# Kernel tuning notes

Measured on AMD Instinct MI355X. Metric: run time of the kernel, lower is better.

Reference implementation:

```python
import jax, jax.numpy as jnp
import numpy as np

NUM_USERS = 50000
NUM_ITEMS = 10000
NUM_SUPPORT = 5
INPUT_DIM = 512
OUTPUT_DIM = 500
NNZ = 400000


def setup_inputs() -> dict:
    key = jax.random.key(0)
    ks = jax.random.split(key, 6)
    x_u = jax.random.normal(ks[0], (NUM_USERS, INPUT_DIM), dtype=jnp.float32)
    x_v = jax.random.normal(ks[1], (NUM_ITEMS, INPUT_DIM), dtype=jnp.float32)
    # random-uniform-like weight init (weight_variable_random_uniform)
    weights_u = jax.random.normal(ks[2], (INPUT_DIM, OUTPUT_DIM), dtype=jnp.float32) * 0.05
    sup_vals = jax.random.uniform(ks[3], (NUM_SUPPORT, NNZ), dtype=jnp.float32)
    sup_rows = jax.random.randint(ks[4], (NUM_SUPPORT, NNZ), 0, NUM_USERS, dtype=jnp.int32)
    sup_cols = jax.random.randint(ks[5], (NUM_SUPPORT, NNZ), 0, NUM_ITEMS, dtype=jnp.int32)
    return {"x_u": x_u, "x_v": x_v, "weights_u": weights_u,
            "sup_vals": sup_vals, "sup_rows": sup_rows, "sup_cols": sup_cols}


def reference(x_u, x_v, weights_u, sup_vals, sup_rows, sup_cols):
    # share_user_item_weights=True -> weights_v is weights_u; dropout=0.0 -> identity.
    hidden = OUTPUT_DIM // NUM_SUPPORT  # 100
    supports_u, supports_v = [], []
    for i in range(NUM_SUPPORT):
        Wi = jax.lax.dynamic_slice_in_dim(weights_u, i * hidden, hidden, axis=1)
        tmp_u = x_u @ Wi  # [num_users, hidden]
        tmp_v = x_v @ Wi  # [num_items, hidden]
        vals = sup_vals[i][:, None]  # [nnz, 1]
        rows, cols = sup_rows[i], sup_cols[i]
        # support_i @ tmp_v  (sparse [U,I] times dense [I,h])
        su = jax.ops.segment_sum(vals * tmp_v[cols], rows, num_segments=NUM_USERS)
        # support_i^T @ tmp_u (sparse [I,U] times dense [U,h])
        sv = jax.ops.segment_sum(vals * tmp_u[rows], cols, num_segments=NUM_ITEMS)
        supports_u.append(su)
        supports_v.append(sv)
    z_u = jnp.concatenate(supports_u, axis=1)  # [num_users, output_dim]
    z_v = jnp.concatenate(supports_v, axis=1)  # [num_items, output_dim]
    return (jax.nn.relu(z_u), jax.nn.relu(z_v))
```

## Files before the change

### kernel.cpp

```cpp
#include <hip/hip_runtime.h>

#define NUM_USERS   50000
#define NUM_ITEMS   10000
#define NUM_SUPPORT 5
#define INPUT_DIM   512
#define OUTPUT_DIM  500
#define NPAD        512
#define HIDDEN      100
#define HPAD        128
#define NNZ         400000
#define NEDGE       (NUM_SUPPORT * NNZ)

#define CH_E        8192
#define NCHUNK      ((NEDGE + CH_E - 1) / CH_E)
#define NB_U        ((NUM_SUPPORT * NUM_USERS + 255) / 256)
#define NB_V        ((NUM_SUPPORT * NUM_ITEMS + 255) / 256)
#define HISTM_U_SZ  (NB_U * NCHUNK)
#define HISTM_U_PAD 239366
#define HISTM_V_SZ  (NB_V * NCHUNK)

typedef unsigned int u32;
typedef unsigned short ushort_t;
typedef __attribute__((ext_vector_type(4))) float f32x4;
typedef __attribute__((ext_vector_type(8))) short bf16x8;

#define GLDS(g, l) __builtin_amdgcn_global_load_lds( \
    (const __attribute__((address_space(1))) unsigned int*)(g), \
    (__attribute__((address_space(3))) unsigned int*)(l), 16, 0, 0)

__device__ inline ushort_t bf16_rne(float f) {
    u32 u = __float_as_uint(f);
    u32 r = (u + 0x7FFFu + ((u >> 16) & 1u)) >> 16;
    return (ushort_t)r;
}
__device__ inline float bf16_lo_f32(u32 w) { return __uint_as_float(w << 16); }
__device__ inline float bf16_hi_f32(u32 w) { return __uint_as_float(w & 0xFFFF0000u); }

__global__ __launch_bounds__(256) void cvt_bf16(
    const float4* __restrict__ in, ushort4* __restrict__ out, int n4)
{
    int t = blockIdx.x * 256 + threadIdx.x;
    if (t >= n4) return;
    float4 v = in[t];
    ushort4 o;
    o.x = bf16_rne(v.x); o.y = bf16_rne(v.y);
    o.z = bf16_rne(v.z); o.w = bf16_rne(v.w);
    out[t] = o;
}

__global__ __launch_bounds__(256) void make_WbT(
    const float* __restrict__ W, ushort_t* __restrict__ WbT)
{
    int t = blockIdx.x * 256 + threadIdx.x;
    int n = t >> 9, k = t & 511;
    float v = (n < OUTPUT_DIM) ? W[k * OUTPUT_DIM + n] : 0.f;
    WbT[t] = bf16_rne(v);
}

#define BM 128
#define BN 128
#define BK 32

__global__ __launch_bounds__(256) void gemm_mfma_bf16(
    const ushort_t* __restrict__ A,
    const ushort_t* __restrict__ BT,
    ushort_t* __restrict__ Xp,
    int M)
{
    const int K = INPUT_DIM;
    __shared__ ushort_t As[BM * BK];
    __shared__ ushort_t Bs[BN * BK];

    const int tid  = threadIdx.x;
    const int wave = tid >> 6;
    const int lane = tid & 63;
    const int quad = lane >> 4;
    const int lr   = lane & 15;
    const int m0 = blockIdx.x * BM;
    const int n0 = blockIdx.y * BN;
    const int wm = (wave >> 1) * 64;
    const int wn = (wave & 1) * 64;

    f32x4 acc[4][4] = {};

    for (int k0 = 0; k0 < K; k0 += BK) {
        #pragma unroll
        for (int h = 0; h < 2; ++h) {
            int o   = tid * 16 + h * 4096;
            int row = o >> 6;
            int byt = o & 63;
            int gr  = m0 + row; if (gr >= M) gr = M - 1;
            GLDS((const char*)A + ((long long)gr * K + k0) * 2 + byt, (char*)As + o);
        }
        #pragma unroll
        for (int h = 0; h < 2; ++h) {
            int o   = tid * 16 + h * 4096;
            int row = o >> 6;
            int byt = o & 63;
            GLDS((const char*)BT + ((long long)(n0 + row) * K + k0) * 2 + byt, (char*)Bs + o);
        }
        asm volatile("s_waitcnt vmcnt(0)" ::: "memory");
        __syncthreads();

        bf16x8 af[4], bfr[4];
        #pragma unroll
        for (int tm = 0; tm < 4; ++tm)
            af[tm] = *(const bf16x8*)(As + (wm + tm * 16 + lr) * BK + quad * 8);
        #pragma unroll
        for (int tn = 0; tn < 4; ++tn)
            bfr[tn] = *(const bf16x8*)(Bs + (wn + tn * 16 + lr) * BK + quad * 8);
        #pragma unroll
        for (int tm = 0; tm < 4; ++tm)
            #pragma unroll
            for (int tn = 0; tn < 4; ++tn)
                acc[tm][tn] = __builtin_amdgcn_mfma_f32_16x16x32_bf16(
                    af[tm], bfr[tn], acc[tm][tn], 0, 0, 0);
        __syncthreads();
    }

    #pragma unroll
    for (int tm = 0; tm < 4; ++tm) {
        int rbase = m0 + wm + tm * 16 + quad * 4;
        #pragma unroll
        for (int tn = 0; tn < 4; ++tn) {
            int col = n0 + wn + tn * 16 + lr;
            if (col >= OUTPUT_DIM) continue;
            int seg = col / HIDDEN;
            int off = col - seg * HIDDEN;
            ushort_t* dst = Xp + (long long)seg * M * HPAD + off;
            #pragma unroll
            for (int g = 0; g < 4; ++g) {
                int row = rbase + g;
                if (row < M) dst[(long long)row * HPAD] = bf16_rne(acc[tm][tn][g]);
            }
        }
    }
}

__global__ __launch_bounds__(256) void scan1(u32* __restrict__ data, int n,
                                             u32* __restrict__ partials)
{
    __shared__ u32 sh[256];
    int t = threadIdx.x;
    int base = blockIdx.x * 1024 + t * 4;
    u32 x[4];
    #pragma unroll
    for (int k = 0; k < 4; ++k) {
        int idx = base + k;
        x[k] = (idx < n) ? data[idx] : 0u;
    }
    u32 tsum = x[0] + x[1] + x[2] + x[3];
    sh[t] = tsum;
    __syncthreads();
    for (int off = 1; off < 256; off <<= 1) {
        u32 v = (t >= off) ? sh[t - off] : 0u;
        __syncthreads();
        sh[t] += v;
        __syncthreads();
    }
    u32 run = (t > 0) ? sh[t - 1] : 0u;
    if (t == 255) partials[blockIdx.x] = sh[255];
    #pragma unroll
    for (int k = 0; k < 4; ++k) {
        int idx = base + k;
        if (idx < n) data[idx] = run;
        run += x[k];
    }
}

__global__ __launch_bounds__(256) void scan_partials(u32* __restrict__ partials, int n)
{
    __shared__ u32 sh[256];
    int t = threadIdx.x;
    u32 x = (t < n) ? partials[t] : 0u;
    sh[t] = x;
    __syncthreads();
    for (int off = 1; off < 256; off <<= 1) {
        u32 v = (t >= off) ? sh[t - off] : 0u;
        __syncthreads();
        sh[t] += v;
        __syncthreads();
    }
    if (t < n) partials[t] = (t > 0) ? sh[t - 1] : 0u;
}

__global__ __launch_bounds__(256) void scan_add(u32* __restrict__ data, int n,
                                                const u32* __restrict__ partials)
{
    int idx = blockIdx.x * 256 + threadIdx.x;
    if (idx < n) data[idx] += partials[idx >> 10];
}

__global__ __launch_bounds__(256) void hist_uv(
    const int* __restrict__ rows, const int* __restrict__ cols,
    u32* __restrict__ histm_u, u32* __restrict__ histm_v)
{
    __shared__ u32 hu[NB_U];
    __shared__ u32 hv[NB_V];
    const int tid = threadIdx.x;
    const int c = blockIdx.x;
    for (int b = tid; b < NB_U; b += 256) hu[b] = 0u;
    for (int b = tid; b < NB_V; b += 256) hv[b] = 0u;
    __syncthreads();
    int base = c * CH_E;
    int end = base + CH_E; if (end > NEDGE) end = NEDGE;
    for (int e = base + tid; e < end; e += 256) {
        unsigned i = (unsigned)e / (unsigned)NNZ;
        u32 ku = i * (u32)NUM_USERS + (u32)rows[e];
        u32 kv = i * (u32)NUM_ITEMS + (u32)cols[e];
        atomicAdd(&hu[ku >> 8], 1u);
        atomicAdd(&hv[kv >> 8], 1u);
    }
    __syncthreads();
    for (int b = tid; b < NB_U; b += 256) histm_u[b * NCHUNK + c] = hu[b];
    for (int b = tid; b < NB_V; b += 256) histm_v[b * NCHUNK + c] = hv[b];
}

template<int NROWS, int GSHIFT>
__global__ __launch_bounds__(256) void partition_edges(
    const int* __restrict__ keyidx, const int* __restrict__ gidx,
    const float* __restrict__ vals,
    const u32* __restrict__ histm, uint2* __restrict__ buf)
{
    constexpr int NKEY = NUM_SUPPORT * NROWS;
    constexpr int NB = (NKEY + 255) / 256;
    __shared__ u32 cur[NB];
    const int tid = threadIdx.x;
    const int c = blockIdx.x;
    for (int b = tid; b < NB; b += 256) cur[b] = histm[b * NCHUNK + c];
    __syncthreads();
    int base = c * CH_E;
    int end = base + CH_E; if (end > NEDGE) end = NEDGE;
    for (int e = base + tid; e < end; e += 256) {
        unsigned i = (unsigned)e / (unsigned)NNZ;
        u32 key = i * (u32)NROWS + (u32)keyidx[e];
        u32 p = atomicAdd(&cur[key >> 8], 1u);
        uint2 pay;
        pay.x = __float_as_uint(vals[e]);
        pay.y = (key << GSHIFT) | (u32)gidx[e];
        buf[p] = pay;
    }
}

template<int NROWS, int GSHIFT>
__global__ __launch_bounds__(256) void bucket_scatter(
    const uint2* __restrict__ buf, const u32* __restrict__ histm,
    u32* __restrict__ ptr, uint2* __restrict__ perm)
{
    constexpr int NKEY = NUM_SUPPORT * NROWS;
    constexpr int NB = (NKEY + 255) / 256;
    __shared__ u32 cnt[256];
    __shared__ u32 scn[256];
    const int tid = threadIdx.x;
    const int b = blockIdx.x;
    const u32 key0 = (u32)b << 8;
    const u32 start = histm[b * NCHUNK];
    const u32 bend  = (b + 1 < NB) ? histm[(b + 1) * NCHUNK] : (u32)NEDGE;
    if (b == 0 && tid == 0) ptr[NKEY] = (u32)NEDGE;
    cnt[tid] = 0u;
    __syncthreads();
    for (u32 j = start + tid; j < bend; j += 256) {
        u32 key = buf[j].y >> GSHIFT;
        atomicAdd(&cnt[key - key0], 1u);
    }
    __syncthreads();
    scn[tid] = cnt[tid];
    __syncthreads();
    for (int off = 1; off < 256; off <<= 1) {
        u32 v = (tid >= off) ? scn[tid - off] : 0u;
        __syncthreads();
        scn[tid] += v;
        __syncthreads();
    }
    u32 myoff = start + scn[tid] - cnt[tid];
    if (key0 + (u32)tid < (u32)NKEY) ptr[key0 + tid] = myoff;
    __syncthreads();
    cnt[tid] = myoff;
    __syncthreads();
    for (u32 j = start + tid; j < bend; j += 256) {
        uint2 q = buf[j];
        u32 key = q.y >> GSHIFT;
        u32 p = atomicAdd(&cnt[key - key0], 1u);
        uint2 out;
        out.x = q.x;
        out.y = q.y & ((1u << GSHIFT) - 1u);
        perm[p] = out;
    }
}

template<int NROWS>
__global__ __launch_bounds__(256) void spmm_pack4(
    const u32* __restrict__ ptr,
    const uint2* __restrict__ perm,
    const ushort_t* __restrict__ Xp,
    float* __restrict__ Z,
    int nsrc)
{
    constexpr int NKEY = NUM_SUPPORT * NROWS;
    int w = (int)((blockIdx.x * 256u + threadIdx.x) >> 6);
    w = __builtin_amdgcn_readfirstlane(w);
    if (w * 4 >= NKEY) return;
    const int lane = threadIdx.x & 63;
    const int g  = lane >> 4;
    const int sl = lane & 15;

    int key = w * 4 + g;
    bool live = key < NKEY;
    int kc = live ? key : (NKEY - 1);
    int i = kc / NROWS;
    int r = kc - i * NROWS;
    u32 s = ptr[kc];
    u32 e = live ? ptr[kc + 1] : s;

    const ushort_t* Xs = Xp + (long long)i * nsrc * HPAD + sl * 8;

    u32 cnt = e - s;
    u32 m = cnt;
    { u32 t = (u32)__shfl_xor((int)m, 16); m = m > t ? m : t; }
    { u32 t = (u32)__shfl_xor((int)m, 32); m = m > t ? m : t; }
    int iters = (int)((m + 1) >> 1);

    float a0 = 0.f, a1 = 0.f, a2 = 0.f, a3 = 0.f;
    float a4 = 0.f, a5 = 0.f, a6 = 0.f, a7 = 0.f;
    u32 k = s;
    for (int it = 0; it < iters; ++it) {
        bool p0 = k < e, p1 = (k + 1) < e;
        u32 j0 = p0 ? k : 0u;
        u32 j1 = p1 ? (k + 1) : 0u;
        uint2 q0 = perm[j0], q1 = perm[j1];
        float v0 = p0 ? __uint_as_float(q0.x) : 0.f;
        float v1 = p1 ? __uint_as_float(q1.x) : 0.f;
        uint4 w0 = *(const uint4*)(Xs + ((long long)q0.y << 7));
        uint4 w1 = *(const uint4*)(Xs + ((long long)q1.y << 7));
        a0 += v0 * bf16_lo_f32(w0.x) + v1 * bf16_lo_f32(w1.x);
        a1 += v0 * bf16_hi_f32(w0.x) + v1 * bf16_hi_f32(w1.x);
        a2 += v0 * bf16_lo_f32(w0.y) + v1 * bf16_lo_f32(w1.y);
        a3 += v0 * bf16_hi_f32(w0.y) + v1 * bf16_hi_f32(w1.y);
        a4 += v0 * bf16_lo_f32(w0.z) + v1 * bf16_lo_f32(w1.z);
        a5 += v0 * bf16_hi_f32(w0.z) + v1 * bf16_hi_f32(w1.z);
        a6 += v0 * bf16_lo_f32(w0.w) + v1 * bf16_lo_f32(w1.w);
        a7 += v0 * bf16_hi_f32(w0.w) + v1 * bf16_hi_f32(w1.w);
        k += 2;
    }

    if (live && sl < 13) {
        float* zp = Z + (long long)r * OUTPUT_DIM + i * HIDDEN + sl * 8;
        float4 o0;
        o0.x = a0 > 0.f ? a0 : 0.f;
        o0.y = a1 > 0.f ? a1 : 0.f;
        o0.z = a2 > 0.f ? a2 : 0.f;
        o0.w = a3 > 0.f ? a3 : 0.f;
        *(float4*)zp = o0;
        if (sl < 12) {
            float4 o1;
            o1.x = a4 > 0.f ? a4 : 0.f;
            o1.y = a5 > 0.f ? a5 : 0.f;
            o1.z = a6 > 0.f ? a6 : 0.f;
            o1.w = a7 > 0.f ? a7 : 0.f;
            *(float4*)(zp + 4) = o1;
        }
    }
}

#define TM 64
#define TN 64
#define TK 16

__global__ __launch_bounds__(256) void gemm_f32(
    const float* __restrict__ A, const float* __restrict__ B,
    float* __restrict__ C, int M, int N, int K, int ldc)
{
    __shared__ float Asl[TK][TM + 4];
    __shared__ float Bsl[TK][TN + 4];
    const int tid = threadIdx.x;
    const int tx  = tid & 15;
    const int ty  = tid >> 4;
    const int row0 = blockIdx.x * TM;
    const int col0 = blockIdx.y * TN;
    float acc[4][4] = {};
    for (int k0 = 0; k0 < K; k0 += TK) {
        #pragma unroll
        for (int it = 0; it < (TM * TK) / 256; ++it) {
            int idx = tid + it * 256;
            int m = idx >> 4, kk = idx & 15, gr = row0 + m;
            Asl[kk][m] = (gr < M) ? A[(long long)gr * K + (k0 + kk)] : 0.f;
        }
        #pragma unroll
        for (int it = 0; it < (TK * TN) / 256; ++it) {
            int idx = tid + it * 256;
            int kk = idx >> 6, n = idx & 63, gc = col0 + n;
            Bsl[kk][n] = (gc < N) ? B[(long long)(k0 + kk) * N + gc] : 0.f;
        }
        __syncthreads();
        #pragma unroll
        for (int kk = 0; kk < TK; ++kk) {
            float a[4], b[4];
            #pragma unroll
            for (int u = 0; u < 4; ++u) a[u] = Asl[kk][ty * 4 + u];
            #pragma unroll
            for (int v = 0; v < 4; ++v) b[v] = Bsl[kk][tx * 4 + v];
            #pragma unroll
            for (int u = 0; u < 4; ++u)
                #pragma unroll
                for (int v = 0; v < 4; ++v)
                    acc[u][v] += a[u] * b[v];
        }
        __syncthreads();
    }
    #pragma unroll
    for (int u = 0; u < 4; ++u) {
        int gr = row0 + ty * 4 + u;
        if (gr >= M) continue;
        #pragma unroll
        for (int v = 0; v < 4; ++v) {
            int gc = col0 + tx * 4 + v;
            if (gc < N) C[(long long)gr * ldc + gc] = acc[u][v];
        }
    }
}

__global__ __launch_bounds__(256) void scatter_edges(
    const float* __restrict__ sup_vals,
    const int*   __restrict__ sup_rows,
    const int*   __restrict__ sup_cols,
    const float* __restrict__ XU, const float* __restrict__ XV,
    float* __restrict__ z_u, float* __restrict__ z_v)
{
    const unsigned t = blockIdx.x * 256u + threadIdx.x;
    const unsigned total = (unsigned)NEDGE * HIDDEN;
    if (t >= total) return;
    const unsigned j  = t % HIDDEN;
    const unsigned eg = t / HIDDEN;
    const unsigned i  = eg / NNZ;
    const float val = sup_vals[eg];
    const int   r   = sup_rows[eg];
    const int   c   = sup_cols[eg];
    const int   colOff = i * HIDDEN + j;
    atomicAdd(&z_u[(long long)r * OUTPUT_DIM + colOff],
              val * XV[(long long)c * NPAD + colOff]);
    atomicAdd(&z_v[(long long)c * OUTPUT_DIM + colOff],
              val * XU[(long long)r * NPAD + colOff]);
}

__global__ __launch_bounds__(256) void relu_inplace(float4* __restrict__ p, int n4)
{
    int t = blockIdx.x * 256 + threadIdx.x;
    if (t >= n4) return;
    float4 v = p[t];
    v.x = v.x > 0.f ? v.x : 0.f;
    v.y = v.y > 0.f ? v.y : 0.f;
    v.z = v.z > 0.f ? v.z : 0.f;
    v.w = v.w > 0.f ? v.w : 0.f;
    p[t] = v;
}

extern "C" void kernel_launch(void* const* d_in, const int* in_sizes, int n_in,
                              void* d_out, int out_size, void* d_ws, size_t ws_size,
                              hipStream_t stream)
{
    const float* x_u      = (const float*)d_in[0];
    const float* x_v      = (const float*)d_in[1];
    const float* W        = (const float*)d_in[2];
    const float* sup_vals = (const float*)d_in[3];
    const int*   sup_rows = (const int*)d_in[4];
    const int*   sup_cols = (const int*)d_in[5];

    float* z_u = (float*)d_out;
    float* z_v = z_u + (long long)NUM_USERS * OUTPUT_DIM;

    const long long NU = (long long)NUM_USERS * 512;
    const long long NV = (long long)NUM_ITEMS * 512;
    const long long PU = (long long)NUM_SUPPORT * NUM_USERS * HPAD;
    const long long PV = (long long)NUM_SUPPORT * NUM_ITEMS * HPAD;
    const int NRU = NUM_SUPPORT * NUM_USERS;
    const int NRV = NUM_SUPPORT * NUM_ITEMS;

    ushort_t* Xp_u  = (ushort_t*)d_ws;
    ushort_t* Xp_v  = Xp_u + PU;
    ushort_t* xu_in = Xp_v + PV;
    ushort_t* xv_in = xu_in + NU;
    ushort_t* WbT   = xv_in + NV;
    u32* row_ptr_u  = (u32*)(WbT + 512 * 512);
    u32* col_ptr_v  = row_ptr_u + (NRU + 1);
    u32* partials   = col_ptr_v + (NRV + 1);
    size_t need_full = ((char*)(partials + 1024)) - ((char*)d_ws);

    uint2* buf      = (uint2*)xu_in;
    u32*   histm_u  = (u32*)(buf + NEDGE);
    u32*   histm_v  = histm_u + HISTM_U_PAD;
    uint2* perm_u   = (uint2*)(histm_v + HISTM_V_SZ);
    uint2* perm_v   = perm_u + NEDGE;

    dim3 blk(256);

    if (ws_size >= need_full) {
        cvt_bf16<<<(int)((NU / 4 + 255) / 256), blk, 0, stream>>>(
            (const float4*)x_u, (ushort4*)xu_in, (int)(NU / 4));
        cvt_bf16<<<(int)((NV / 4 + 255) / 256), blk, 0, stream>>>(
            (const float4*)x_v, (ushort4*)xv_in, (int)(NV / 4));
        make_WbT<<<(512 * 512) / 256, blk, 0, stream>>>(W, WbT);
        gemm_mfma_bf16<<<dim3((NUM_USERS + BM - 1) / BM, 512 / BN), blk, 0, stream>>>(
            xu_in, WbT, Xp_u, NUM_USERS);
        gemm_mfma_bf16<<<dim3((NUM_ITEMS + BM - 1) / BM, 512 / BN), blk, 0, stream>>>(
            xv_in, WbT, Xp_v, NUM_ITEMS);

        auto scan_u32 = [&](u32* data, int n) {
            int nb = (n + 1023) / 1024;
            scan1<<<nb, blk, 0, stream>>>(data, n, partials);
            scan_partials<<<1, blk, 0, stream>>>(partials, nb);
            scan_add<<<(n + 255) / 256, blk, 0, stream>>>(data, n, partials);
        };

        hist_uv<<<NCHUNK, blk, 0, stream>>>(sup_rows, sup_cols, histm_u, histm_v);

        scan_u32(histm_u, HISTM_U_SZ);
        partition_edges<NUM_USERS, 14><<<NCHUNK, blk, 0, stream>>>(
            sup_rows, sup_cols, sup_vals, histm_u, buf);
        bucket_scatter<NUM_USERS, 14><<<NB_U, blk, 0, stream>>>(
            buf, histm_u, row_ptr_u, perm_u);

        scan_u32(histm_v, HISTM_V_SZ);
        partition_edges<NUM_ITEMS, 16><<<NCHUNK, blk, 0, stream>>>(
            sup_cols, sup_rows, sup_vals, histm_v, buf);
        bucket_scatter<NUM_ITEMS, 16><<<NB_V, blk, 0, stream>>>(
            buf, histm_v, col_ptr_v, perm_v);

        spmm_pack4<NUM_USERS><<<((NRU / 4) * 64) / 256, blk, 0, stream>>>(
            row_ptr_u, perm_u, Xp_v, z_u, NUM_ITEMS);
        spmm_pack4<NUM_ITEMS><<<((NRV / 4) * 64) / 256, blk, 0, stream>>>(
            col_ptr_v, perm_v, Xp_u, z_v, NUM_USERS);
    } else {
        float* XU = (float*)d_ws;
        float* XV = XU + (long long)NUM_USERS * NPAD;
        gemm_f32<<<dim3((NUM_USERS + TM - 1) / TM, (OUTPUT_DIM + TN - 1) / TN),
                   blk, 0, stream>>>(x_u, W, XU, NUM_USERS, OUTPUT_DIM, INPUT_DIM, NPAD);
        gemm_f32<<<dim3((NUM_ITEMS + TM - 1) / TM, (OUTPUT_DIM + TN - 1) / TN),
                   blk, 0, stream>>>(x_v, W, XV, NUM_ITEMS, OUTPUT_DIM, INPUT_DIM, NPAD);
        hipMemsetAsync(d_out, 0, (size_t)out_size * sizeof(float), stream);
        unsigned total = (unsigned)NEDGE * HIDDEN;
        scatter_edges<<<(total + 255u) / 256u, blk, 0, stream>>>(
            sup_vals, sup_rows, sup_cols, XU, XV, z_u, z_v);
        int n4 = out_size / 4;
        relu_inplace<<<(n4 + 255) / 256, blk, 0, stream>>>((float4*)d_out, n4);
    }
}
```

Before: 568.3 us.

## Merge user/item sort pipelines into joint scan, partition and scatter kernels

```diff
diff --git a/kernel.cpp b/kernel.cpp
--- a/kernel.cpp
+++ b/kernel.cpp
@@ -16,8 +16,9 @@
 #define NB_U        ((NUM_SUPPORT * NUM_USERS + 255) / 256)
 #define NB_V        ((NUM_SUPPORT * NUM_ITEMS + 255) / 256)
 #define HISTM_U_SZ  (NB_U * NCHUNK)
-#define HISTM_U_PAD 239366
+#define HISTM_U_ALIGN 239616
 #define HISTM_V_SZ  (NB_V * NCHUNK)
+#define HISTM_TOT   (HISTM_U_ALIGN + HISTM_V_SZ)
 
 typedef unsigned int u32;
 typedef unsigned short ushort_t;
@@ -36,16 +37,21 @@
 __device__ inline float bf16_lo_f32(u32 w) { return __uint_as_float(w << 16); }
 __device__ inline float bf16_hi_f32(u32 w) { return __uint_as_float(w & 0xFFFF0000u); }
 
-__global__ __launch_bounds__(256) void cvt_bf16(
-    const float4* __restrict__ in, ushort4* __restrict__ out, int n4)
+__global__ __launch_bounds__(256) void cvt_bf16_2(
+    const float4* __restrict__ a, const float4* __restrict__ b,
+    ushort4* __restrict__ oa, ushort4* __restrict__ ob, int na4, int nb4)
 {
     int t = blockIdx.x * 256 + threadIdx.x;
-    if (t >= n4) return;
-    float4 v = in[t];
+    const float4* src;
+    ushort4* dst;
+    int idx;
+    if (t < na4) { src = a; dst = oa; idx = t; }
+    else { idx = t - na4; if (idx >= nb4) return; src = b; dst = ob; }
+    float4 v = src[idx];
     ushort4 o;
     o.x = bf16_rne(v.x); o.y = bf16_rne(v.y);
     o.z = bf16_rne(v.z); o.w = bf16_rne(v.w);
-    out[t] = o;
+    dst[idx] = o;
 }
 
 __global__ __launch_bounds__(256) void make_WbT(
@@ -168,14 +174,14 @@
     }
 }
 
-__global__ __launch_bounds__(256) void scan_partials(u32* __restrict__ partials, int n)
-{
-    __shared__ u32 sh[256];
+__global__ __launch_bounds__(512) void scan_partials(u32* __restrict__ partials, int n)
+{
+    __shared__ u32 sh[512];
     int t = threadIdx.x;
     u32 x = (t < n) ? partials[t] : 0u;
     sh[t] = x;
     __syncthreads();
-    for (int off = 1; off < 256; off <<= 1) {
+    for (int off = 1; off < 512; off <<= 1) {
         u32 v = (t >= off) ? sh[t - off] : 0u;
         __syncthreads();
         sh[t] += v;
@@ -188,7 +194,9 @@
                                                 const u32* __restrict__ partials)
 {
     int idx = blockIdx.x * 256 + threadIdx.x;
-    if (idx < n) data[idx] += partials[idx >> 10];
+    if (idx >= n) return;
+    u32 adj = (idx >= HISTM_U_ALIGN) ? (u32)NEDGE : 0u;
+    data[idx] = data[idx] + partials[idx >> 10] - adj;
 }
 
 __global__ __launch_bounds__(256) void hist_uv(
@@ -199,6 +207,8 @@
     __shared__ u32 hv[NB_V];
     const int tid = threadIdx.x;
     const int c = blockIdx.x;
+    if (c == 0)
+        for (int z = HISTM_U_SZ + tid; z < HISTM_U_ALIGN; z += 256) histm_u[z] = 0u;
     for (int b = tid; b < NB_U; b += 256) hu[b] = 0u;
     for (int b = tid; b < NB_V; b += 256) hv[b] = 0u;
     __syncthreads();
@@ -216,43 +226,46 @@
     for (int b = tid; b < NB_V; b += 256) histm_v[b * NCHUNK + c] = hv[b];
 }
 
-template<int NROWS, int GSHIFT>
-__global__ __launch_bounds__(256) void partition_edges(
-    const int* __restrict__ keyidx, const int* __restrict__ gidx,
+__global__ __launch_bounds__(256) void partition_uv(
+    const int* __restrict__ rows, const int* __restrict__ cols,
     const float* __restrict__ vals,
-    const u32* __restrict__ histm, uint2* __restrict__ buf)
-{
-    constexpr int NKEY = NUM_SUPPORT * NROWS;
-    constexpr int NB = (NKEY + 255) / 256;
-    __shared__ u32 cur[NB];
+    const u32* __restrict__ histm_u, const u32* __restrict__ histm_v,
+    uint2* __restrict__ buf_u, uint2* __restrict__ buf_v)
+{
+    __shared__ u32 cu[NB_U];
+    __shared__ u32 cv[NB_V];
     const int tid = threadIdx.x;
     const int c = blockIdx.x;
-    for (int b = tid; b < NB; b += 256) cur[b] = histm[b * NCHUNK + c];
+    for (int b = tid; b < NB_U; b += 256) cu[b] = histm_u[b * NCHUNK + c];
+    for (int b = tid; b < NB_V; b += 256) cv[b] = histm_v[b * NCHUNK + c];
     __syncthreads();
     int base = c * CH_E;
     int end = base + CH_E; if (end > NEDGE) end = NEDGE;
     for (int e = base + tid; e < end; e += 256) {
         unsigned i = (unsigned)e / (unsigned)NNZ;
-        u32 key = i * (u32)NROWS + (u32)keyidx[e];
-        u32 p = atomicAdd(&cur[key >> 8], 1u);
-        uint2 pay;
-        pay.x = __float_as_uint(vals[e]);
-        pay.y = (key << GSHIFT) | (u32)gidx[e];
-        buf[p] = pay;
+        int r = rows[e];
+        int col = cols[e];
+        u32 vb = __float_as_uint(vals[e]);
+        u32 ku = i * (u32)NUM_USERS + (u32)r;
+        u32 kv = i * (u32)NUM_ITEMS + (u32)col;
+        u32 pu = atomicAdd(&cu[ku >> 8], 1u);
+        uint2 eu; eu.x = vb; eu.y = (ku << 14) | (u32)col;
+        buf_u[pu] = eu;
+        u32 pv = atomicAdd(&cv[kv >> 8], 1u);
+        uint2 ev; ev.x = vb; ev.y = (kv << 16) | (u32)r;
+        buf_v[pv] = ev;
     }
 }
 
 template<int NROWS, int GSHIFT>
-__global__ __launch_bounds__(256) void bucket_scatter(
-    const uint2* __restrict__ buf, const u32* __restrict__ histm,
-    u32* __restrict__ ptr, uint2* __restrict__ perm)
+__device__ inline void bucket_body(
+    int b, const uint2* __restrict__ buf, const u32* __restrict__ histm,
+    u32* __restrict__ ptr, uint2* __restrict__ perm,
+    u32* cnt, u32* scn)
 {
     constexpr int NKEY = NUM_SUPPORT * NROWS;
     constexpr int NB = (NKEY + 255) / 256;
-    __shared__ u32 cnt[256];
-    __shared__ u32 scn[256];
     const int tid = threadIdx.x;
-    const int b = blockIdx.x;
     const u32 key0 = (u32)b << 8;
     const u32 start = histm[b * NCHUNK];
     const u32 bend  = (b + 1 < NB) ? histm[(b + 1) * NCHUNK] : (u32)NEDGE;
@@ -288,6 +301,20 @@
     }
 }
 
+__global__ __launch_bounds__(256) void bucket_scatter_uv(
+    const uint2* __restrict__ buf_u, const u32* __restrict__ histm_u,
+    u32* __restrict__ ptr_u, uint2* __restrict__ perm_u,
+    const uint2* __restrict__ buf_v, const u32* __restrict__ histm_v,
+    u32* __restrict__ ptr_v, uint2* __restrict__ perm_v)
+{
+    __shared__ u32 cnt[256];
+    __shared__ u32 scn[256];
+    if (blockIdx.x < NB_U)
+        bucket_body<NUM_USERS, 14>(blockIdx.x, buf_u, histm_u, ptr_u, perm_u, cnt, scn);
+    else
+        bucket_body<NUM_ITEMS, 16>(blockIdx.x - NB_U, buf_v, histm_v, ptr_v, perm_v, cnt, scn);
+}
+
 template<int NROWS>
 __global__ __launch_bounds__(256) void spmm_pack4(
     const u32* __restrict__ ptr,
@@ -305,45 +332,56 @@
     const int sl = lane & 15;
 
     int key = w * 4 + g;
-    bool live = key < NKEY;
-    int kc = live ? key : (NKEY - 1);
-    int i = kc / NROWS;
-    int r = kc - i * NROWS;
-    u32 s = ptr[kc];
-    u32 e = live ? ptr[kc + 1] : s;
+    int i = key / NROWS;
+    int r = key - i * NROWS;
+    u32 s = ptr[key];
+    u32 e = ptr[key + 1];
 
     const ushort_t* Xs = Xp + (long long)i * nsrc * HPAD + sl * 8;
 
-    u32 cnt = e - s;
-    u32 m = cnt;
+    u32 m = e - s;
     { u32 t = (u32)__shfl_xor((int)m, 16); m = m > t ? m : t; }
     { u32 t = (u32)__shfl_xor((int)m, 32); m = m > t ? m : t; }
-    int iters = (int)((m + 1) >> 1);
+    int iters = (int)((m + 3) >> 2);
 
     float a0 = 0.f, a1 = 0.f, a2 = 0.f, a3 = 0.f;
     float a4 = 0.f, a5 = 0.f, a6 = 0.f, a7 = 0.f;
     u32 k = s;
     for (int it = 0; it < iters; ++it) {
-        bool p0 = k < e, p1 = (k + 1) < e;
+        bool p0 = k < e, p1 = (k + 1) < e, p2 = (k + 2) < e, p3 = (k + 3) < e;
         u32 j0 = p0 ? k : 0u;
         u32 j1 = p1 ? (k + 1) : 0u;
-        uint2 q0 = perm[j0], q1 = perm[j1];
+        u32 j2 = p2 ? (k + 2) : 0u;
+        u32 j3 = p3 ? (k + 3) : 0u;
+        uint2 q0 = perm[j0], q1 = perm[j1], q2 = perm[j2], q3 = perm[j3];
         float v0 = p0 ? __uint_as_float(q0.x) : 0.f;
         float v1 = p1 ? __uint_as_float(q1.x) : 0.f;
+        float v2 = p2 ? __uint_as_float(q2.x) : 0.f;
+        float v3 = p3 ? __uint_as_float(q3.x) : 0.f;
         uint4 w0 = *(const uint4*)(Xs + ((long long)q0.y << 7));
         uint4 w1 = *(const uint4*)(Xs + ((long long)q1.y << 7));
-        a0 += v0 * bf16_lo_f32(w0.x) + v1 * bf16_lo_f32(w1.x);
-        a1 += v0 * bf16_hi_f32(w0.x) + v1 * bf16_hi_f32(w1.x);
-        a2 += v0 * bf16_lo_f32(w0.y) + v1 * bf16_lo_f32(w1.y);
-        a3 += v0 * bf16_hi_f32(w0.y) + v1 * bf16_hi_f32(w1.y);
-        a4 += v0 * bf16_lo_f32(w0.z) + v1 * bf16_lo_f32(w1.z);
-        a5 += v0 * bf16_hi_f32(w0.z) + v1 * bf16_hi_f32(w1.z);
-        a6 += v0 * bf16_lo_f32(w0.w) + v1 * bf16_lo_f32(w1.w);
-        a7 += v0 * bf16_hi_f32(w0.w) + v1 * bf16_hi_f32(w1.w);
-        k += 2;
-    }
-
-    if (live && sl < 13) {
+        uint4 w2 = *(const uint4*)(Xs + ((long long)q2.y << 7));
+        uint4 w3 = *(const uint4*)(Xs + ((long long)q3.y << 7));
+        a0 += v0 * bf16_lo_f32(w0.x) + v1 * bf16_lo_f32(w1.x)
+            + v2 * bf16_lo_f32(w2.x) + v3 * bf16_lo_f32(w3.x);
+        a1 += v0 * bf16_hi_f32(w0.x) + v1 * bf16_hi_f32(w1.x)
+            + v2 * bf16_hi_f32(w2.x) + v3 * bf16_hi_f32(w3.x);
+        a2 += v0 * bf16_lo_f32(w0.y) + v1 * bf16_lo_f32(w1.y)
+            + v2 * bf16_lo_f32(w2.y) + v3 * bf16_lo_f32(w3.y);
+        a3 += v0 * bf16_hi_f32(w0.y) + v1 * bf16_hi_f32(w1.y)
+            + v2 * bf16_hi_f32(w2.y) + v3 * bf16_hi_f32(w3.y);
+        a4 += v0 * bf16_lo_f32(w0.z) + v1 * bf16_lo_f32(w1.z)
+            + v2 * bf16_lo_f32(w2.z) + v3 * bf16_lo_f32(w3.z);
+        a5 += v0 * bf16_hi_f32(w0.z) + v1 * bf16_hi_f32(w1.z)
+            + v2 * bf16_hi_f32(w2.z) + v3 * bf16_hi_f32(w3.z);
+        a6 += v0 * bf16_lo_f32(w0.w) + v1 * bf16_lo_f32(w1.w)
+            + v2 * bf16_lo_f32(w2.w) + v3 * bf16_lo_f32(w3.w);
+        a7 += v0 * bf16_hi_f32(w0.w) + v1 * bf16_hi_f32(w1.w)
+            + v2 * bf16_hi_f32(w2.w) + v3 * bf16_hi_f32(w3.w);
+        k += 4;
+    }
+
+    if (sl < 13) {
         float* zp = Z + (long long)r * OUTPUT_DIM + i * HIDDEN + sl * 8;
         float4 o0;
         o0.x = a0 > 0.f ? a0 : 0.f;
@@ -483,47 +521,46 @@
     u32* row_ptr_u  = (u32*)(WbT + 512 * 512);
     u32* col_ptr_v  = row_ptr_u + (NRU + 1);
     u32* partials   = col_ptr_v + (NRV + 1);
-    size_t need_full = ((char*)(partials + 1024)) - ((char*)d_ws);
-
-    uint2* buf      = (uint2*)xu_in;
-    u32*   histm_u  = (u32*)(buf + NEDGE);
-    u32*   histm_v  = histm_u + HISTM_U_PAD;
+    size_t need_full = ((char*)(partials + 512)) - ((char*)d_ws);
+
+    uint2* buf_v    = (uint2*)xu_in;
+    u32*   histm_u  = (u32*)(buf_v + NEDGE);
+    u32*   histm_v  = histm_u + HISTM_U_ALIGN;
     uint2* perm_u   = (uint2*)(histm_v + HISTM_V_SZ);
     uint2* perm_v   = perm_u + NEDGE;
+    uint2* buf_u    = (uint2*)z_u;
 
     dim3 blk(256);
 
     if (ws_size >= need_full) {
-        cvt_bf16<<<(int)((NU / 4 + 255) / 256), blk, 0, stream>>>(
-            (const float4*)x_u, (ushort4*)xu_in, (int)(NU / 4));
-        cvt_bf16<<<(int)((NV / 4 + 255) / 256), blk, 0, stream>>>(
-            (const float4*)x_v, (ushort4*)xv_in, (int)(NV / 4));
+        {
+            int na4 = (int)(NU / 4), nb4 = (int)(NV / 4);
+            cvt_bf16_2<<<(na4 + nb4 + 255) / 256, blk, 0, stream>>>(
+                (const float4*)x_u, (const float4*)x_v,
+                (ushort4*)xu_in, (ushort4*)xv_in, na4, nb4);
+        }
         make_WbT<<<(512 * 512) / 256, blk, 0, stream>>>(W, WbT);
         gemm_mfma_bf16<<<dim3((NUM_USERS + BM - 1) / BM, 512 / BN), blk, 0, stream>>>(
             xu_in, WbT, Xp_u, NUM_USERS);
         gemm_mfma_bf16<<<dim3((NUM_ITEMS + BM - 1) / BM, 512 / BN), blk, 0, stream>>>(
             xv_in, WbT, Xp_v, NUM_ITEMS);
 
-        auto scan_u32 = [&](u32* data, int n) {
-            int nb = (n + 1023) / 1024;
-            scan1<<<nb, blk, 0, stream>>>(data, n, partials);
-            scan_partials<<<1, blk, 0, stream>>>(partials, nb);
-            scan_add<<<(n + 255) / 256, blk, 0, stream>>>(data, n, partials);
-        };
-
         hist_uv<<<NCHUNK, blk, 0, stream>>>(sup_rows, sup_cols, histm_u, histm_v);
 
-        scan_u32(histm_u, HISTM_U_SZ);
-        partition_edges<NUM_USERS, 14><<<NCHUNK, blk, 0, stream>>>(
-            sup_rows, sup_cols, sup_vals, histm_u, buf);
-        bucket_scatter<NUM_USERS, 14><<<NB_U, blk, 0, stream>>>(
-            buf, histm_u, row_ptr_u, perm_u);
-
-        scan_u32(histm_v, HISTM_V_SZ);
-        partition_edges<NUM_ITEMS, 16><<<NCHUNK, blk, 0, stream>>>(
-            sup_cols, sup_rows, sup_vals, histm_v, buf);
-        bucket_scatter<NUM_ITEMS, 16><<<NB_V, blk, 0, stream>>>(
-            buf, histm_v, col_ptr_v, perm_v);
+        {
+            int nb = (HISTM_TOT + 1023) / 1024;
+            scan1<<<nb, blk, 0, stream>>>(histm_u, HISTM_TOT, partials);
+            scan_partials<<<1, dim3(512), 0, stream>>>(partials, nb);
+            scan_add<<<(HISTM_TOT + 255) / 256, blk, 0, stream>>>(
+                histm_u, HISTM_TOT, partials);
+        }
+
+        partition_uv<<<NCHUNK, blk, 0, stream>>>(
+            sup_rows, sup_cols, sup_vals, histm_u, histm_v, buf_u, buf_v);
+
+        bucket_scatter_uv<<<NB_U + NB_V, blk, 0, stream>>>(
+            buf_u, histm_u, row_ptr_u, perm_u,
+            buf_v, histm_v, col_ptr_v, perm_v);
 
         spmm_pack4<NUM_USERS><<<((NRU / 4) * 64) / 256, blk, 0, stream>>>(
             row_ptr_u, perm_u, Xp_v, z_u, NUM_ITEMS);
```

Result: faster. 519.2 us (-8.6%).
